# Optimization experiments

Hardware: AMD Instinct MI355X
Metric: run time of the kernel (lower is better)

The kernel has to match this reference:

```python
import jax, jax.numpy as jnp
import numpy as np

EPS = 1e-5
ALPHA = 0.1
STEPS = 2


def setup_inputs() -> dict:
    key = jax.random.key(0)
    k1, k2 = jax.random.split(key)
    B, S, n, d = 4, 4096, 4, 1024
    streams = jax.random.normal(k1, (B, S, n, d), dtype=jnp.float32)
    norm_scale = jnp.ones((n * d,), dtype=jnp.float32)
    # matches nn.init.normal_(std=0.01) on Linear weight, zero bias
    proj_w = jax.random.normal(k2, (3 * n * n, n * d), dtype=jnp.float32) * 0.01
    proj_b = jnp.zeros((3 * n * n,), dtype=jnp.float32)
    out_scale = jnp.ones((1,), dtype=jnp.float32) * 0.1
    return {"streams": streams, "norm_scale": norm_scale, "proj_w": proj_w,
            "proj_b": proj_b, "out_scale": out_scale}


def _cayley_iterative(H_raw, alpha=ALPHA, steps=STEPS):
    # Skew-symmetrize then fixed-point iterate toward Cayley transform.
    W = H_raw - jnp.swapaxes(H_raw, -2, -1)          # [B,S,n,n]
    I = jnp.eye(W.shape[-1], dtype=W.dtype)           # broadcasts over [B,S]
    Y = I + alpha * W
    for _ in range(steps):
        Y = I + (alpha / 2) * jnp.matmul(W, I + Y)
    return Y


def reference(streams, norm_scale, proj_w, proj_b, out_scale):
    B, S, n, d = streams.shape
    # --- _compute_matrices (shared by aggregate & distribute; same values) ---
    x = streams.reshape(B, S, n * d)
    rms = jnp.sqrt(jnp.mean(x * x, axis=-1, keepdims=True) + EPS)
    raw = (x / rms * norm_scale) @ proj_w.T + proj_b  # [B,S,3*n*n]
    raw = raw.reshape(B, S, 3, n, n)
    H_pre = jax.nn.softmax(raw[:, :, 0], axis=-1)     # row-stochastic
    H_post = jax.nn.softmax(raw[:, :, 1], axis=-2)    # column-stochastic
    H_res = _cayley_iterative(raw[:, :, 2])           # ~orthogonal [B,S,n,n]
    # --- aggregate: mix streams, mean over stream axis ---
    h_new = jnp.matmul(H_pre, streams).mean(axis=2)   # [B,S,d]
    # --- distribute: orthogonal residual + scaled broadcast of layer output ---
    residual = jnp.matmul(H_res, streams)             # [B,S,n,d]
    h_b = jnp.broadcast_to(h_new[:, :, None, :], streams.shape)
    output = jnp.matmul(H_post, h_b)                  # [B,S,n,d]
    return residual + out_scale * output
```

## Files before the change

### kernel.cpp

```cpp
#include <hip/hip_runtime.h>
#include <hip/hip_bf16.h>

#define EPS_F 1e-5f

typedef __bf16 bf16x8 __attribute__((ext_vector_type(8)));
typedef float f32x4 __attribute__((ext_vector_type(4)));

static __device__ __forceinline__ unsigned int pack_bf16x2(float a, float b) {
    union { float f; unsigned int u; } ca, cb;
    ca.f = a; cb.f = b;
    unsigned int ua = (ca.u + 0x7fffu + ((ca.u >> 16) & 1u)) >> 16;
    unsigned int ub = (cb.u + 0x7fffu + ((cb.u >> 16) & 1u)) >> 16;
    return ua | (ub << 16);
}

__global__ void scale_weights(const float* __restrict__ w,
                              const float* __restrict__ ns,
                              unsigned int* __restrict__ wbf)
{
    const int i = (blockIdx.x * 256 + threadIdx.x) * 4;
    const float4 wv = *reinterpret_cast<const float4*>(w + i);
    const float4 nv = *reinterpret_cast<const float4*>(ns + (i & 4095));
    uint2 o;
    o.x = pack_bf16x2(wv.x * nv.x, wv.y * nv.y);
    o.y = pack_bf16x2(wv.z * nv.z, wv.w * nv.w);
    *reinterpret_cast<uint2*>(wbf + (i >> 1)) = o;
}

__global__ __launch_bounds__(512)
void compute_M(const float* __restrict__ streams,
               const unsigned short* __restrict__ wbf,
               const float* __restrict__ proj_b,
               const float* __restrict__ out_scale,
               float* __restrict__ Mout)
{
    __shared__ float red[8][3][16][16];
    __shared__ float ssq_red[8][16];

    const int tid  = threadIdx.x;
    const int wv   = tid >> 6;
    const int lane = tid & 63;
    const size_t tok0 = (size_t)blockIdx.x * 16;

    {
        const int r = lane & 15;
        const int g = lane >> 4;
        const int koff = g * 8;
        const int kbase = wv * 512;

        const float* ap = streams + (tok0 + r) * 4096 + kbase + koff;
        const unsigned short* wp = wbf + (size_t)r * 4096 + kbase + koff;

        f32x4 acc0 = {0.f, 0.f, 0.f, 0.f};
        f32x4 acc1 = acc0, acc2 = acc0;
        float ssq = 0.f;

        bf16x8 pb0 = *reinterpret_cast<const bf16x8*>(wp);
        bf16x8 pb1 = *reinterpret_cast<const bf16x8*>(wp + 16 * 4096);
        bf16x8 pb2 = *reinterpret_cast<const bf16x8*>(wp + 32 * 4096);

        #pragma unroll 1
        for (int p = 0; p < 2; ++p) {
            f32x4 ar[16];
            #pragma unroll
            for (int q = 0; q < 8; ++q) {
                ar[2 * q]     = *reinterpret_cast<const f32x4*>(ap + (p * 8 + q) * 32);
                ar[2 * q + 1] = *reinterpret_cast<const f32x4*>(ap + (p * 8 + q) * 32 + 4);
            }
            __builtin_amdgcn_sched_barrier(0);

            #pragma unroll
            for (int q = 0; q < 8; ++q) {
                const int ks = p * 8 + q;
                const bf16x8 b0 = pb0, b1 = pb1, b2 = pb2;
                if (ks < 15) {
                    pb0 = *reinterpret_cast<const bf16x8*>(wp + (ks + 1) * 32);
                    pb1 = *reinterpret_cast<const bf16x8*>(wp + 16 * 4096 + (ks + 1) * 32);
                    pb2 = *reinterpret_cast<const bf16x8*>(wp + 32 * 4096 + (ks + 1) * 32);
                }
                const f32x4 a0 = ar[2 * q], a1 = ar[2 * q + 1];
                ssq = fmaf(a0[0], a0[0], ssq); ssq = fmaf(a0[1], a0[1], ssq);
                ssq = fmaf(a0[2], a0[2], ssq); ssq = fmaf(a0[3], a0[3], ssq);
                ssq = fmaf(a1[0], a1[0], ssq); ssq = fmaf(a1[1], a1[1], ssq);
                ssq = fmaf(a1[2], a1[2], ssq); ssq = fmaf(a1[3], a1[3], ssq);
                bf16x8 a;
                a[0] = (__bf16)a0[0]; a[1] = (__bf16)a0[1]; a[2] = (__bf16)a0[2]; a[3] = (__bf16)a0[3];
                a[4] = (__bf16)a1[0]; a[5] = (__bf16)a1[1]; a[6] = (__bf16)a1[2]; a[7] = (__bf16)a1[3];
                acc0 = __builtin_amdgcn_mfma_f32_16x16x32_bf16(a, b0, acc0, 0, 0, 0);
                acc1 = __builtin_amdgcn_mfma_f32_16x16x32_bf16(a, b1, acc1, 0, 0, 0);
                acc2 = __builtin_amdgcn_mfma_f32_16x16x32_bf16(a, b2, acc2, 0, 0, 0);
            }
        }

        ssq += __shfl_xor(ssq, 16, 64);
        ssq += __shfl_xor(ssq, 32, 64);
        if (lane < 16) ssq_red[wv][lane] = ssq;

        #pragma unroll
        for (int rr = 0; rr < 4; ++rr) {
            red[wv][0][g * 4 + rr][r] = acc0[rr];
            red[wv][1][g * 4 + rr][r] = acc1[rr];
            red[wv][2][g * 4 + rr][r] = acc2[rr];
        }
    }
    __syncthreads();

    const int t = wv * 2 + (lane >> 5);
    float Mr[16];
    {
        float st = 0.f;
        #pragma unroll
        for (int kp = 0; kp < 8; ++kp) st += ssq_red[kp][t];
        const float invr = rsqrtf(st * (1.f / 4096.f) + EPS_F);

        #define REDUCE_TILE(tile, raw)                                             \
            {                                                                      \
                _Pragma("unroll")                                                  \
                for (int c4 = 0; c4 < 4; ++c4) {                                   \
                    f32x4 s = {0.f, 0.f, 0.f, 0.f};                                \
                    _Pragma("unroll")                                              \
                    for (int kp = 0; kp < 8; ++kp)                                 \
                        s += *reinterpret_cast<const f32x4*>(&red[kp][tile][t][c4 * 4]); \
                    const float4 pb = *reinterpret_cast<const float4*>(&proj_b[tile * 16 + c4 * 4]); \
                    raw[c4*4 + 0] = s[0] * invr + pb.x;                            \
                    raw[c4*4 + 1] = s[1] * invr + pb.y;                            \
                    raw[c4*4 + 2] = s[2] * invr + pb.z;                            \
                    raw[c4*4 + 3] = s[3] * invr + pb.w;                            \
                }                                                                  \
            }

        float c[4] = {0.f, 0.f, 0.f, 0.f};
        {
            float raw[16];
            REDUCE_TILE(0, raw)
            #pragma unroll
            for (int i = 0; i < 4; ++i) {
                const float a0 = raw[i*4+0], a1 = raw[i*4+1], a2 = raw[i*4+2], a3 = raw[i*4+3];
                const float m = fmaxf(fmaxf(a0, a1), fmaxf(a2, a3));
                const float e0 = expf(a0 - m), e1 = expf(a1 - m);
                const float e2 = expf(a2 - m), e3 = expf(a3 - m);
                const float inv = 1.f / (e0 + e1 + e2 + e3);
                c[0] = fmaf(e0, inv, c[0]); c[1] = fmaf(e1, inv, c[1]);
                c[2] = fmaf(e2, inv, c[2]); c[3] = fmaf(e3, inv, c[3]);
            }
            c[0] *= 0.25f; c[1] *= 0.25f; c[2] *= 0.25f; c[3] *= 0.25f;
        }

        float rs[4] = {0.f, 0.f, 0.f, 0.f};
        {
            float raw[16];
            REDUCE_TILE(1, raw)
            #pragma unroll
            for (int j = 0; j < 4; ++j) {
                const float b0 = raw[j], b1 = raw[4+j], b2 = raw[8+j], b3 = raw[12+j];
                const float m = fmaxf(fmaxf(b0, b1), fmaxf(b2, b3));
                const float e0 = expf(b0 - m), e1 = expf(b1 - m);
                const float e2 = expf(b2 - m), e3 = expf(b3 - m);
                const float inv = 1.f / (e0 + e1 + e2 + e3);
                rs[0] = fmaf(e0, inv, rs[0]); rs[1] = fmaf(e1, inv, rs[1]);
                rs[2] = fmaf(e2, inv, rs[2]); rs[3] = fmaf(e3, inv, rs[3]);
            }
        }

        float W[16], Y[16];
        {
            float raw[16];
            REDUCE_TILE(2, raw)
            #pragma unroll
            for (int i = 0; i < 4; ++i)
                #pragma unroll
                for (int j = 0; j < 4; ++j)
                    W[i*4+j] = raw[i*4+j] - raw[j*4+i];
        }
        #pragma unroll
        for (int i = 0; i < 16; ++i) Y[i] = 0.1f * W[i];
        Y[0] += 1.f; Y[5] += 1.f; Y[10] += 1.f; Y[15] += 1.f;
        #pragma unroll
        for (int it = 0; it < 2; ++it) {
            float T1[16];
            #pragma unroll
            for (int i = 0; i < 16; ++i) T1[i] = Y[i];
            T1[0] += 1.f; T1[5] += 1.f; T1[10] += 1.f; T1[15] += 1.f;
            float Yn[16];
            #pragma unroll
            for (int i = 0; i < 4; ++i)
                #pragma unroll
                for (int j = 0; j < 4; ++j) {
                    float s = W[i*4+0] * T1[0*4+j];
                    s = fmaf(W[i*4+1], T1[1*4+j], s);
                    s = fmaf(W[i*4+2], T1[2*4+j], s);
                    s = fmaf(W[i*4+3], T1[3*4+j], s);
                    Yn[i*4+j] = ((i == j) ? 1.f : 0.f) + 0.05f * s;
                }
            #pragma unroll
            for (int i = 0; i < 16; ++i) Y[i] = Yn[i];
        }

        const float os = out_scale[0];
        #pragma unroll
        for (int i = 0; i < 4; ++i)
            #pragma unroll
            for (int j = 0; j < 4; ++j)
                Mr[i*4+j] = Y[i*4+j] + os * rs[i] * c[j];
        #undef REDUCE_TILE
    }

    if ((lane & 31) == 0) {
        float* mp = Mout + (tok0 + t) * 16;
        *reinterpret_cast<float4*>(mp +  0) = make_float4(Mr[0],  Mr[1],  Mr[2],  Mr[3]);
        *reinterpret_cast<float4*>(mp +  4) = make_float4(Mr[4],  Mr[5],  Mr[6],  Mr[7]);
        *reinterpret_cast<float4*>(mp +  8) = make_float4(Mr[8],  Mr[9],  Mr[10], Mr[11]);
        *reinterpret_cast<float4*>(mp + 12) = make_float4(Mr[12], Mr[13], Mr[14], Mr[15]);
    }
}

static __device__ __forceinline__ f32x4 mix4(float4 m, f32x4 x0, f32x4 x1,
                                             f32x4 x2, f32x4 x3) {
    f32x4 o;
    #pragma unroll
    for (int e = 0; e < 4; ++e)
        o[e] = fmaf(m.w, x3[e], fmaf(m.z, x2[e], fmaf(m.y, x1[e], m.x * x0[e])));
    return o;
}

__global__ __launch_bounds__(256)
void apply_M(const float* __restrict__ streams,
             const float* __restrict__ Mfull,
             float* __restrict__ out)
{
    const size_t t = blockIdx.x;
    const int c = threadIdx.x * 4;

    const float4* mp = reinterpret_cast<const float4*>(Mfull + t * 16);
    const float4 m0 = mp[0], m1 = mp[1], m2 = mp[2], m3 = mp[3];

    const float* src = streams + t * 4096;
    float* dst = out + t * 4096;

    const f32x4 x0 = *reinterpret_cast<const f32x4*>(src + c);
    const f32x4 x1 = *reinterpret_cast<const f32x4*>(src + 1024 + c);
    const f32x4 x2 = *reinterpret_cast<const f32x4*>(src + 2048 + c);
    const f32x4 x3 = *reinterpret_cast<const f32x4*>(src + 3072 + c);

    __builtin_nontemporal_store(mix4(m0, x0, x1, x2, x3),
                                reinterpret_cast<f32x4*>(dst + c));
    __builtin_nontemporal_store(mix4(m1, x0, x1, x2, x3),
                                reinterpret_cast<f32x4*>(dst + 1024 + c));
    __builtin_nontemporal_store(mix4(m2, x0, x1, x2, x3),
                                reinterpret_cast<f32x4*>(dst + 2048 + c));
    __builtin_nontemporal_store(mix4(m3, x0, x1, x2, x3),
                                reinterpret_cast<f32x4*>(dst + 3072 + c));
}

extern "C" void kernel_launch(void* const* d_in, const int* in_sizes, int n_in,
                              void* d_out, int out_size, void* d_ws, size_t ws_size,
                              hipStream_t stream) {
    const float* streams    = (const float*)d_in[0];
    const float* norm_scale = (const float*)d_in[1];
    const float* proj_w     = (const float*)d_in[2];
    const float* proj_b     = (const float*)d_in[3];
    const float* out_scale  = (const float*)d_in[4];
    float* outp = (float*)d_out;

    unsigned int* wbf = (unsigned int*)d_ws;
    float* Mfull = (float*)((char*)d_ws + 393216);

    scale_weights<<<dim3(192), 256, 0, stream>>>(proj_w, norm_scale, wbf);

    const int n_tok = in_sizes[0] / 4096;
    compute_M<<<dim3(n_tok / 16), 512, 0, stream>>>(streams,
                                                    (const unsigned short*)wbf,
                                                    proj_b, out_scale, Mfull);
    apply_M<<<dim3(n_tok), 256, 0, stream>>>(streams, Mfull, outp);
}
```

Measured before the change: 175.4 us.

## Fuse per-token mixing matrix application into the compute_M kernel

Merges the apply_M kernel into compute_M so each block applies its freshly computed 4x4 mixing matrices to its own 16 tokens. Each half-wave handles one token and streams the 4x1024 slab in eight column chunks, prefetching the next chunk while computing the current one. This removes one kernel launch and the write and re-read of the M buffer, and the streams slab may still be in cache from the projection pass. In exchange, the output phase now runs with only 1024 blocks of 512 threads, each doing serial chunk loops, which may expose less memory-level parallelism than the separate 16K-block apply kernel.

Result: faster. 155.5 us (-11.4%).

```diff
diff --git a/kernel.cpp b/kernel.cpp
--- a/kernel.cpp
+++ b/kernel.cpp
@@ -28,11 +28,11 @@
 }
 
 __global__ __launch_bounds__(512)
-void compute_M(const float* __restrict__ streams,
-               const unsigned short* __restrict__ wbf,
-               const float* __restrict__ proj_b,
-               const float* __restrict__ out_scale,
-               float* __restrict__ Mout)
+void fused_stream_mix(const float* __restrict__ streams,
+                      const unsigned short* __restrict__ wbf,
+                      const float* __restrict__ proj_b,
+                      const float* __restrict__ out_scale,
+                      float* __restrict__ out)
 {
     __shared__ float red[8][3][16][16];
     __shared__ float ssq_red[8][16];
@@ -105,7 +105,16 @@
     }
     __syncthreads();
 
-    const int t = wv * 2 + (lane >> 5);
+    const int t  = wv * 2 + (lane >> 5);
+    const int l5 = lane & 31;
+    const float* src = streams + (tok0 + t) * 4096;
+    float* dst = out + (tok0 + t) * 4096;
+
+    f32x4 px0 = *reinterpret_cast<const f32x4*>(src + l5 * 4);
+    f32x4 px1 = *reinterpret_cast<const f32x4*>(src + 1024 + l5 * 4);
+    f32x4 px2 = *reinterpret_cast<const f32x4*>(src + 2048 + l5 * 4);
+    f32x4 px3 = *reinterpret_cast<const f32x4*>(src + 3072 + l5 * 4);
+
     float Mr[16];
     {
         float st = 0.f;
@@ -205,51 +214,28 @@
         #undef REDUCE_TILE
     }
 
-    if ((lane & 31) == 0) {
-        float* mp = Mout + (tok0 + t) * 16;
-        *reinterpret_cast<float4*>(mp +  0) = make_float4(Mr[0],  Mr[1],  Mr[2],  Mr[3]);
-        *reinterpret_cast<float4*>(mp +  4) = make_float4(Mr[4],  Mr[5],  Mr[6],  Mr[7]);
-        *reinterpret_cast<float4*>(mp +  8) = make_float4(Mr[8],  Mr[9],  Mr[10], Mr[11]);
-        *reinterpret_cast<float4*>(mp + 12) = make_float4(Mr[12], Mr[13], Mr[14], Mr[15]);
+    #pragma unroll 2
+    for (int cq = 0; cq < 8; ++cq) {
+        const f32x4 x0 = px0, x1 = px1, x2 = px2, x3 = px3;
+        if (cq < 7) {
+            const int ncol = (cq + 1) * 128 + l5 * 4;
+            px0 = *reinterpret_cast<const f32x4*>(src + ncol);
+            px1 = *reinterpret_cast<const f32x4*>(src + 1024 + ncol);
+            px2 = *reinterpret_cast<const f32x4*>(src + 2048 + ncol);
+            px3 = *reinterpret_cast<const f32x4*>(src + 3072 + ncol);
+        }
+        const int col = cq * 128 + l5 * 4;
+        #pragma unroll
+        for (int i = 0; i < 4; ++i) {
+            f32x4 o;
+            #pragma unroll
+            for (int e = 0; e < 4; ++e)
+                o[e] = fmaf(Mr[i*4+3], x3[e],
+                        fmaf(Mr[i*4+2], x2[e],
+                          fmaf(Mr[i*4+1], x1[e], Mr[i*4+0] * x0[e])));
+            __builtin_nontemporal_store(o, reinterpret_cast<f32x4*>(dst + i * 1024 + col));
+        }
     }
-}
-
-static __device__ __forceinline__ f32x4 mix4(float4 m, f32x4 x0, f32x4 x1,
-                                             f32x4 x2, f32x4 x3) {
-    f32x4 o;
-    #pragma unroll
-    for (int e = 0; e < 4; ++e)
-        o[e] = fmaf(m.w, x3[e], fmaf(m.z, x2[e], fmaf(m.y, x1[e], m.x * x0[e])));
-    return o;
-}
-
-__global__ __launch_bounds__(256)
-void apply_M(const float* __restrict__ streams,
-             const float* __restrict__ Mfull,
-             float* __restrict__ out)
-{
-    const size_t t = blockIdx.x;
-    const int c = threadIdx.x * 4;
-
-    const float4* mp = reinterpret_cast<const float4*>(Mfull + t * 16);
-    const float4 m0 = mp[0], m1 = mp[1], m2 = mp[2], m3 = mp[3];
-
-    const float* src = streams + t * 4096;
-    float* dst = out + t * 4096;
-
-    const f32x4 x0 = *reinterpret_cast<const f32x4*>(src + c);
-    const f32x4 x1 = *reinterpret_cast<const f32x4*>(src + 1024 + c);
-    const f32x4 x2 = *reinterpret_cast<const f32x4*>(src + 2048 + c);
-    const f32x4 x3 = *reinterpret_cast<const f32x4*>(src + 3072 + c);
-
-    __builtin_nontemporal_store(mix4(m0, x0, x1, x2, x3),
-                                reinterpret_cast<f32x4*>(dst + c));
-    __builtin_nontemporal_store(mix4(m1, x0, x1, x2, x3),
-                                reinterpret_cast<f32x4*>(dst + 1024 + c));
-    __builtin_nontemporal_store(mix4(m2, x0, x1, x2, x3),
-                                reinterpret_cast<f32x4*>(dst + 2048 + c));
-    __builtin_nontemporal_store(mix4(m3, x0, x1, x2, x3),
-                                reinterpret_cast<f32x4*>(dst + 3072 + c));
 }
 
 extern "C" void kernel_launch(void* const* d_in, const int* in_sizes, int n_in,
@@ -263,13 +249,11 @@
     float* outp = (float*)d_out;
 
     unsigned int* wbf = (unsigned int*)d_ws;
-    float* Mfull = (float*)((char*)d_ws + 393216);
 
     scale_weights<<<dim3(192), 256, 0, stream>>>(proj_w, norm_scale, wbf);
 
     const int n_tok = in_sizes[0] / 4096;
-    compute_M<<<dim3(n_tok / 16), 512, 0, stream>>>(streams,
-                                                    (const unsigned short*)wbf,
-                                                    proj_b, out_scale, Mfull);
-    apply_M<<<dim3(n_tok), 256, 0, stream>>>(streams, Mfull, outp);
-}
+    fused_stream_mix<<<dim3(n_tok / 16), 512, 0, stream>>>(streams,
+                                                           (const unsigned short*)wbf,
+                                                           proj_b, out_scale, outp);
+}
```
